# Kernel optimization log

Measured on AMD Instinct MI355X. Metric: run time of the kernel, lower is better.

## Reference

```python
import jax, jax.numpy as jnp
import numpy as np

B, LX, LY, D = 8, 128, 512, 256


def setup_inputs() -> dict:
    key = jax.random.key(0)
    k = jax.random.split(key, 7)
    s1 = 1.0 / np.sqrt(2 * D)
    s2 = 1.0 / np.sqrt(D)
    return {
        "x": jax.random.normal(k[0], (B, LX, D), dtype=jnp.float32),
        "y": jax.random.normal(k[1], (B, LY, D), dtype=jnp.float32),
        "y_mask": jax.random.randint(k[2], (B, LY), 0, 2).astype(bool),
        "W1": jax.random.uniform(k[3], (2 * D, D), jnp.float32, -s1, s1),
        "b1": jax.random.uniform(k[4], (D,), jnp.float32, -s1, s1),
        "W2": jax.random.uniform(k[5], (D, 1), jnp.float32, -s2, s2),
        "b2": jax.random.uniform(k[6], (1,), jnp.float32, -s2, s2),
    }


def reference(x, y, y_mask, W1, b1, W2, b2):
    # Algebraically split the first linear on the concat [x; y]:
    # cat([x,y]) @ W1 == x @ W1[:D] + y @ W1[D:]
    d = x.shape[-1]
    hx = jnp.einsum('bxd,de->bxe', x, W1[:d])            # (B, LX, D)
    hy = jnp.einsum('byd,de->bye', y, W1[d:])            # (B, LY, D)
    h = jax.nn.relu(hx[:, :, None, :] + hy[:, None, :, :] + b1)  # (B, LX, LY, D)
    scores = jnp.einsum('bxyd,d->bxy', h, W2[:, 0]) + b2[0]      # (B, LX, LY)
    scores = jnp.where(y_mask[:, None, :], -jnp.inf, scores)
    weights = jax.nn.softmax(scores, axis=2)
    contexts = jnp.einsum('bxy,byd->bxd', weights, y)    # (B, LX, D)
    return contexts
```

## Files before the change

### kernel.cpp

```cpp
#include <hip/hip_runtime.h>
#include <math.h>

#define BB 8
#define LX 128
#define LY 512
#define DD 256

typedef _Float16 h2t __attribute__((ext_vector_type(2)));

static __device__ __forceinline__ h2t u2h(unsigned int u) {
    h2t r; __builtin_memcpy(&r, &u, 4); return r;
}
static __device__ __forceinline__ unsigned int pk16(float a, float b) {
    h2t h; h.x = (_Float16)a; h.y = (_Float16)b;
    unsigned int u; __builtin_memcpy(&u, &h, 4); return u;
}

#if defined(__has_builtin) && __has_builtin(__builtin_amdgcn_fdot2)
#define DOT2(a, b, c) __builtin_amdgcn_fdot2((a), (b), (c), false)
#else
#define DOT2(a, b, c) fmaf((float)(a).x, (float)(b).x, fmaf((float)(a).y, (float)(b).y, (c)))
#endif

#define A16_OFF  0
#define CT16_OFF 131072
#define W16_OFF  655360
#define PART_OFF 655488
#define PML_OFF  4849792

__global__ __launch_bounds__(256) void gemm_kernel(
    const float* __restrict__ x, const float* __restrict__ y,
    const float* __restrict__ W1, const float* __restrict__ b1,
    const float* __restrict__ W2, float* __restrict__ ws)
{
    __shared__ float sA[32][20];
    __shared__ float sW[32][128];

    const int g  = blockIdx.x;
    const int t  = threadIdx.x;
    const int tc = t & 31;
    const int tr = t >> 5;

    const bool isA = (g < 128);
    const float* inp;
    const float* wbase;
    int row0, col0;
    if (isA) { col0 = (g & 1) * 128;  row0 = (g >> 1) * 16;  inp = x; wbase = W1; }
    else     { int h = g - 128; col0 = (h & 1) * 128; row0 = (h >> 1) * 16; inp = y; wbase = W1 + DD * DD; }

    float acc[2][4];
    #pragma unroll
    for (int i = 0; i < 2; ++i)
        #pragma unroll
        for (int j = 0; j < 4; ++j) acc[i][j] = 0.f;

    for (int k0 = 0; k0 < DD; k0 += 32) {
        __syncthreads();
        if (t < 128) {
            int row = t >> 3, kq = t & 7;
            const float4 v = *(const float4*)(inp + (size_t)(row0 + row) * DD + k0 + 4 * kq);
            sA[4*kq + 0][row] = v.x;
            sA[4*kq + 1][row] = v.y;
            sA[4*kq + 2][row] = v.z;
            sA[4*kq + 3][row] = v.w;
        }
        #pragma unroll
        for (int i = 0; i < 4; ++i) {
            int flat = t + i * 256;
            int kk = flat >> 5, c4 = flat & 31;
            *(float4*)&sW[kk][4*c4] = *(const float4*)(wbase + (size_t)(k0 + kk) * DD + col0 + 4 * c4);
        }
        __syncthreads();
        #pragma unroll
        for (int k = 0; k < 32; ++k) {
            const float a0 = sA[k][2*tr], a1 = sA[k][2*tr + 1];
            const float4 w4 = *(const float4*)&sW[k][4*tc];
            acc[0][0] = fmaf(a0, w4.x, acc[0][0]);
            acc[0][1] = fmaf(a0, w4.y, acc[0][1]);
            acc[0][2] = fmaf(a0, w4.z, acc[0][2]);
            acc[0][3] = fmaf(a0, w4.w, acc[0][3]);
            acc[1][0] = fmaf(a1, w4.x, acc[1][0]);
            acc[1][1] = fmaf(a1, w4.y, acc[1][1]);
            acc[1][2] = fmaf(a1, w4.z, acc[1][2]);
            acc[1][3] = fmaf(a1, w4.w, acc[1][3]);
        }
    }

    const int dq = (col0 >> 2) + tc;
    if (isA) {
        uint2* A16u2 = (uint2*)(ws + A16_OFF);
        const float4 bv = *(const float4*)(b1 + col0 + 4 * tc);
        #pragma unroll
        for (int i = 0; i < 2; ++i) {
            const int r = row0 + 2 * tr + i;
            uint2 st;
            st.x = pk16(acc[i][0] + bv.x, acc[i][1] + bv.y);
            st.y = pk16(acc[i][2] + bv.z, acc[i][3] + bv.w);
            A16u2[((size_t)r * 32 + (dq & 31)) * 2 + (dq >> 5)] = st;
        }
        if (g == 0 && t < 64) {
            uint2* W16u2 = (uint2*)(ws + W16_OFF);
            const float4 wv = *(const float4*)(W2 + 4 * t);
            uint2 st;
            st.x = pk16(wv.x, wv.y);
            st.y = pk16(wv.z, wv.w);
            W16u2[((t & 31)) * 2 + (t >> 5)] = st;
        }
    } else {
        uint2* Ct16u2 = (uint2*)(ws + CT16_OFF);
        #pragma unroll
        for (int i = 0; i < 2; ++i) {
            const int ry = row0 + 2 * tr + i;
            const int bb = ry >> 9, yy = ry & 511;
            uint2 st;
            st.x = pk16(acc[i][0], acc[i][1]);
            st.y = pk16(acc[i][2], acc[i][3]);
            Ct16u2[((size_t)(bb * 64 + dq)) * 512 + yy] = st;
        }
    }
}

__global__ __launch_bounds__(256) void score_kernel(
    const float* __restrict__ yin, const int* __restrict__ ymask,
    const float* __restrict__ b2,
    const uint4* __restrict__ A16, const uint2* __restrict__ Ct,
    const uint4* __restrict__ W16,
    float* __restrict__ part, float* __restrict__ pml)
{
    const int t    = threadIdx.x;
    const int lane = t & 63;
    const int w    = __builtin_amdgcn_readfirstlane(t >> 6);
    const int b    = blockIdx.x & 7;
    const int r2   = blockIdx.x >> 3;
    const int xg   = r2 & 15;
    const int yc   = r2 >> 4;
    const int ylo  = lane & 31;
    const bool hi  = (lane >> 5) != 0;
    const int y    = yc * 128 + w * 32 + ylo;
    const int grow0 = b * LX + xg * 8;

    const uint2* ctp = Ct + ((size_t)(b * 64 + (hi ? 32 : 0))) * 512 + y;
    const uint4* A8  = A16 + (size_t)grow0 * 32;
    const float  b2v = b2[0];

    h2t zz; zz.x = (_Float16)0.f; zz.y = (_Float16)0.f;
    float sA[8], sB[8];
    #pragma unroll
    for (int r = 0; r < 8; ++r) { sA[r] = 0.f; sB[r] = 0.f; }

    #pragma unroll 2
    for (int dqi = 0; dqi < 32; ++dqi) {
        const uint2 cu = ctp[(size_t)dqi * 512];
        const h2t c0 = u2h(cu.x), c1 = u2h(cu.y);
        const uint4 wv = W16[dqi];
        const h2t w0 = u2h(hi ? wv.z : wv.x);
        const h2t w1 = u2h(hi ? wv.w : wv.y);
        #pragma unroll
        for (int r = 0; r < 8; ++r) {
            const uint4 av = A8[r * 32 + dqi];
            const h2t a0 = u2h(hi ? av.z : av.x);
            const h2t a1 = u2h(hi ? av.w : av.y);
            const h2t h0 = __builtin_elementwise_max(a0 + c0, zz);
            const h2t h1 = __builtin_elementwise_max(a1 + c1, zz);
            sA[r] = DOT2(h0, w0, sA[r]);
            sB[r] = DOT2(h1, w1, sB[r]);
        }
    }

    const bool msk = ymask[(size_t)b * LY + y] != 0;
    float p[8]; int pi[8]; float l[8];
    #pragma unroll
    for (int r = 0; r < 8; ++r) {
        float s = sA[r] + sB[r];
        s += __shfl_xor(s, 32);
        p[r] = msk ? 0.f : __expf(s + b2v);
        pi[r] = __float_as_int(p[r]);
        float lv = p[r];
        #pragma unroll
        for (int off = 16; off; off >>= 1) lv += __shfl_xor(lv, off);
        l[r] = lv;
    }

    float4 acc[8];
    #pragma unroll
    for (int r = 0; r < 8; ++r) acc[r] = make_float4(0.f, 0.f, 0.f, 0.f);

    const float4* yb = (const float4*)yin + ((size_t)(b * LY + yc * 128 + w * 32)) * 64 + lane;
    #pragma unroll 4
    for (int yy = 0; yy < 32; ++yy) {
        const float4 v = yb[(size_t)yy * 64];
        #pragma unroll
        for (int r = 0; r < 8; ++r) {
            const float q = __int_as_float(__builtin_amdgcn_readlane(pi[r], yy));
            acc[r].x = fmaf(q, v.x, acc[r].x);
            acc[r].y = fmaf(q, v.y, acc[r].y);
            acc[r].z = fmaf(q, v.z, acc[r].z);
            acc[r].w = fmaf(q, v.w, acc[r].w);
        }
    }

    const size_t pw = (((size_t)(b * 16 + xg) * 4 + yc) * 4 + w);
    float* pb = part + pw * 8 * DD;
    #pragma unroll
    for (int r = 0; r < 8; ++r)
        *(float4*)(pb + (size_t)r * DD + 4 * lane) = acc[r];
    if (lane == 0) {
        #pragma unroll
        for (int r = 0; r < 8; ++r) pml[pw * 8 + r] = l[r];
    }
}

__global__ __launch_bounds__(256) void combine_kernel(
    const float* __restrict__ part, const float* __restrict__ pml,
    float* __restrict__ out)
{
    const int t = threadIdx.x;
    const int b = blockIdx.x & 7;
    const int x = blockIdx.x >> 3;
    const int xg = x >> 3, xi = x & 7;

    float L = 0.f;
    float acc = 0.f;
    #pragma unroll
    for (int c = 0; c < 16; ++c) {
        const size_t idx = (((size_t)(b * 16 + xg) * 4 + (c >> 2)) * 4 + (c & 3)) * 8 + xi;
        L   += pml[idx];
        acc += part[idx * DD + t];
    }
    out[((size_t)(b * LX + x)) * DD + t] = acc / L;
}

extern "C" void kernel_launch(void* const* d_in, const int* in_sizes, int n_in,
                              void* d_out, int out_size, void* d_ws, size_t ws_size,
                              hipStream_t stream) {
    const float* x     = (const float*)d_in[0];
    const float* y     = (const float*)d_in[1];
    const int*   ymask = (const int*)  d_in[2];
    const float* W1    = (const float*)d_in[3];
    const float* b1    = (const float*)d_in[4];
    const float* W2    = (const float*)d_in[5];
    const float* b2    = (const float*)d_in[6];
    float* ws  = (float*)d_ws;
    float* out = (float*)d_out;

    hipLaunchKernelGGL(gemm_kernel, dim3(640), dim3(256), 0, stream, x, y, W1, b1, W2, ws);
    hipLaunchKernelGGL(score_kernel, dim3(512), dim3(256), 0, stream,
                       y, ymask, b2,
                       (const uint4*)(ws + A16_OFF), (const uint2*)(ws + CT16_OFF),
                       (const uint4*)(ws + W16_OFF),
                       ws + PART_OFF, ws + PML_OFF);
    hipLaunchKernelGGL(combine_kernel, dim3(1024), dim3(256), 0, stream,
                       ws + PART_OFF, ws + PML_OFF, out);
}
```

Baseline: 50.41 us.

## Fuse score and combine kernels into one block-per-x-group kernel with LDS softmax weights

Replaces the split score/combine kernels with a single kernel in which each 512-thread block handles 4 query rows against all 512 y positions of one batch. A and W2 values are broadcast with readlane instead of per-row loads, and the A16/W16 layouts are simplified to match. Softmax weights are staged in LDS so the same block computes the weighted sum of y directly. This removes the partial-sum workspace traffic and one kernel launch. In exchange each block does a full-length 512-step reduction over y with 256 blocks, so there is less parallelism and more y reloads per block.

New measurement: 46.08 us. 1.09x faster.

```diff
diff --git a/kernel.cpp b/kernel.cpp
--- a/kernel.cpp
+++ b/kernel.cpp
@@ -14,6 +14,9 @@
 static __device__ __forceinline__ unsigned int pk16(float a, float b) {
     h2t h; h.x = (_Float16)a; h.y = (_Float16)b;
     unsigned int u; __builtin_memcpy(&u, &h, 4); return u;
+}
+static __device__ __forceinline__ h2t rlh(unsigned int v, int l) {
+    return u2h((unsigned int)__builtin_amdgcn_readlane((int)v, l));
 }
 
 #if defined(__has_builtin) && __has_builtin(__builtin_amdgcn_fdot2)
@@ -25,8 +28,6 @@
 #define A16_OFF  0
 #define CT16_OFF 131072
 #define W16_OFF  655360
-#define PART_OFF 655488
-#define PML_OFF  4849792
 
 __global__ __launch_bounds__(256) void gemm_kernel(
     const float* __restrict__ x, const float* __restrict__ y,
@@ -96,7 +97,7 @@
             uint2 st;
             st.x = pk16(acc[i][0] + bv.x, acc[i][1] + bv.y);
             st.y = pk16(acc[i][2] + bv.z, acc[i][3] + bv.w);
-            A16u2[((size_t)r * 32 + (dq & 31)) * 2 + (dq >> 5)] = st;
+            A16u2[(size_t)r * 64 + dq] = st;
         }
         if (g == 0 && t < 64) {
             uint2* W16u2 = (uint2*)(ws + W16_OFF);
@@ -104,7 +105,7 @@
             uint2 st;
             st.x = pk16(wv.x, wv.y);
             st.y = pk16(wv.z, wv.w);
-            W16u2[((t & 31)) * 2 + (t >> 5)] = st;
+            W16u2[t] = st;
         }
     } else {
         uint2* Ct16u2 = (uint2*)(ws + CT16_OFF);
@@ -120,114 +121,109 @@
     }
 }
 
-__global__ __launch_bounds__(256) void score_kernel(
+__global__ __launch_bounds__(512) void fused_kernel(
     const float* __restrict__ yin, const int* __restrict__ ymask,
     const float* __restrict__ b2,
-    const uint4* __restrict__ A16, const uint2* __restrict__ Ct,
-    const uint4* __restrict__ W16,
-    float* __restrict__ part, float* __restrict__ pml)
+    const uint2* __restrict__ A16, const uint2* __restrict__ Ct,
+    const uint2* __restrict__ W16,
+    float* __restrict__ out)
 {
+    __shared__ __align__(16) float pl[LY][4];
+    __shared__ __align__(16) float4 Lp[8];
+
     const int t    = threadIdx.x;
     const int lane = t & 63;
     const int w    = __builtin_amdgcn_readfirstlane(t >> 6);
     const int b    = blockIdx.x & 7;
-    const int r2   = blockIdx.x >> 3;
-    const int xg   = r2 & 15;
-    const int yc   = r2 >> 4;
-    const int ylo  = lane & 31;
-    const bool hi  = (lane >> 5) != 0;
-    const int y    = yc * 128 + w * 32 + ylo;
-    const int grow0 = b * LX + xg * 8;
-
-    const uint2* ctp = Ct + ((size_t)(b * 64 + (hi ? 32 : 0))) * 512 + y;
-    const uint4* A8  = A16 + (size_t)grow0 * 32;
+    const int xg   = blockIdx.x >> 3;
+    const int y    = w * 64 + lane;
+
+    const uint2* Ab = A16 + ((size_t)(b * LX + xg * 4)) * 64;
+    uint2 av0 = Ab[lane];
+    uint2 av1 = Ab[64 + lane];
+    uint2 av2 = Ab[128 + lane];
+    uint2 av3 = Ab[192 + lane];
+    const uint2 wv = W16[lane];
+
+    const uint2* ctb = Ct + ((size_t)b * 64) * 512 + y;
     const float  b2v = b2[0];
-
-    h2t zz; zz.x = (_Float16)0.f; zz.y = (_Float16)0.f;
-    float sA[8], sB[8];
+    const bool   msk = ymask[(size_t)b * LY + y] != 0;
+
+    float s0 = 0.f, s1 = 0.f, s2 = 0.f, s3 = 0.f;
+
+    #pragma unroll 4
+    for (int dq = 0; dq < 64; ++dq) {
+        const uint2 cu = ctb[(size_t)dq * 512];
+        const h2t c0 = u2h(cu.x), c1 = u2h(cu.y);
+        const h2t w0 = rlh(wv.x, dq), w1 = rlh(wv.y, dq);
+        h2t zz; zz.x = (_Float16)0.f; zz.y = (_Float16)0.f;
+        {
+            const h2t a0 = rlh(av0.x, dq), a1 = rlh(av0.y, dq);
+            const h2t h0 = __builtin_elementwise_max(a0 + c0, zz);
+            const h2t h1 = __builtin_elementwise_max(a1 + c1, zz);
+            s0 = DOT2(h0, w0, s0); s0 = DOT2(h1, w1, s0);
+        }
+        {
+            const h2t a0 = rlh(av1.x, dq), a1 = rlh(av1.y, dq);
+            const h2t h0 = __builtin_elementwise_max(a0 + c0, zz);
+            const h2t h1 = __builtin_elementwise_max(a1 + c1, zz);
+            s1 = DOT2(h0, w0, s1); s1 = DOT2(h1, w1, s1);
+        }
+        {
+            const h2t a0 = rlh(av2.x, dq), a1 = rlh(av2.y, dq);
+            const h2t h0 = __builtin_elementwise_max(a0 + c0, zz);
+            const h2t h1 = __builtin_elementwise_max(a1 + c1, zz);
+            s2 = DOT2(h0, w0, s2); s2 = DOT2(h1, w1, s2);
+        }
+        {
+            const h2t a0 = rlh(av3.x, dq), a1 = rlh(av3.y, dq);
+            const h2t h0 = __builtin_elementwise_max(a0 + c0, zz);
+            const h2t h1 = __builtin_elementwise_max(a1 + c1, zz);
+            s3 = DOT2(h0, w0, s3); s3 = DOT2(h1, w1, s3);
+        }
+    }
+
+    const float p0 = msk ? 0.f : __expf(s0 + b2v);
+    const float p1 = msk ? 0.f : __expf(s1 + b2v);
+    const float p2 = msk ? 0.f : __expf(s2 + b2v);
+    const float p3 = msk ? 0.f : __expf(s3 + b2v);
+
+    float l0 = p0, l1 = p1, l2 = p2, l3 = p3;
     #pragma unroll
-    for (int r = 0; r < 8; ++r) { sA[r] = 0.f; sB[r] = 0.f; }
-
-    #pragma unroll 2
-    for (int dqi = 0; dqi < 32; ++dqi) {
-        const uint2 cu = ctp[(size_t)dqi * 512];
-        const h2t c0 = u2h(cu.x), c1 = u2h(cu.y);
-        const uint4 wv = W16[dqi];
-        const h2t w0 = u2h(hi ? wv.z : wv.x);
-        const h2t w1 = u2h(hi ? wv.w : wv.y);
-        #pragma unroll
-        for (int r = 0; r < 8; ++r) {
-            const uint4 av = A8[r * 32 + dqi];
-            const h2t a0 = u2h(hi ? av.z : av.x);
-            const h2t a1 = u2h(hi ? av.w : av.y);
-            const h2t h0 = __builtin_elementwise_max(a0 + c0, zz);
-            const h2t h1 = __builtin_elementwise_max(a1 + c1, zz);
-            sA[r] = DOT2(h0, w0, sA[r]);
-            sB[r] = DOT2(h1, w1, sB[r]);
-        }
-    }
-
-    const bool msk = ymask[(size_t)b * LY + y] != 0;
-    float p[8]; int pi[8]; float l[8];
+    for (int off = 32; off; off >>= 1) {
+        l0 += __shfl_xor(l0, off);
+        l1 += __shfl_xor(l1, off);
+        l2 += __shfl_xor(l2, off);
+        l3 += __shfl_xor(l3, off);
+    }
+
+    *(float4*)&pl[y][0] = make_float4(p0, p1, p2, p3);
+    if (lane == 0) Lp[w] = make_float4(l0, l1, l2, l3);
+    __syncthreads();
+
+    const int d  = t & 255;
+    const int xh = t >> 8;
+    float L0 = 0.f, L1 = 0.f;
     #pragma unroll
-    for (int r = 0; r < 8; ++r) {
-        float s = sA[r] + sB[r];
-        s += __shfl_xor(s, 32);
-        p[r] = msk ? 0.f : __expf(s + b2v);
-        pi[r] = __float_as_int(p[r]);
-        float lv = p[r];
-        #pragma unroll
-        for (int off = 16; off; off >>= 1) lv += __shfl_xor(lv, off);
-        l[r] = lv;
-    }
-
-    float4 acc[8];
-    #pragma unroll
-    for (int r = 0; r < 8; ++r) acc[r] = make_float4(0.f, 0.f, 0.f, 0.f);
-
-    const float4* yb = (const float4*)yin + ((size_t)(b * LY + yc * 128 + w * 32)) * 64 + lane;
-    #pragma unroll 4
-    for (int yy = 0; yy < 32; ++yy) {
-        const float4 v = yb[(size_t)yy * 64];
-        #pragma unroll
-        for (int r = 0; r < 8; ++r) {
-            const float q = __int_as_float(__builtin_amdgcn_readlane(pi[r], yy));
-            acc[r].x = fmaf(q, v.x, acc[r].x);
-            acc[r].y = fmaf(q, v.y, acc[r].y);
-            acc[r].z = fmaf(q, v.z, acc[r].z);
-            acc[r].w = fmaf(q, v.w, acc[r].w);
-        }
-    }
-
-    const size_t pw = (((size_t)(b * 16 + xg) * 4 + yc) * 4 + w);
-    float* pb = part + pw * 8 * DD;
-    #pragma unroll
-    for (int r = 0; r < 8; ++r)
-        *(float4*)(pb + (size_t)r * DD + 4 * lane) = acc[r];
-    if (lane == 0) {
-        #pragma unroll
-        for (int r = 0; r < 8; ++r) pml[pw * 8 + r] = l[r];
-    }
-}
-
-__global__ __launch_bounds__(256) void combine_kernel(
-    const float* __restrict__ part, const float* __restrict__ pml,
-    float* __restrict__ out)
-{
-    const int t = threadIdx.x;
-    const int b = blockIdx.x & 7;
-    const int x = blockIdx.x >> 3;
-    const int xg = x >> 3, xi = x & 7;
-
-    float L = 0.f;
-    float acc = 0.f;
-    #pragma unroll
-    for (int c = 0; c < 16; ++c) {
-        const size_t idx = (((size_t)(b * 16 + xg) * 4 + (c >> 2)) * 4 + (c & 3)) * 8 + xi;
-        L   += pml[idx];
-        acc += part[idx * DD + t];
-    }
-    out[((size_t)(b * LX + x)) * DD + t] = acc / L;
+    for (int ww = 0; ww < 8; ++ww) {
+        const float4 lv = Lp[ww];
+        L0 += xh ? lv.z : lv.x;
+        L1 += xh ? lv.w : lv.y;
+    }
+
+    float a0 = 0.f, a1 = 0.f;
+    const float* Yb = yin + (size_t)b * LY * DD + d;
+    #pragma unroll 8
+    for (int yy = 0; yy < LY; ++yy) {
+        const float v = Yb[(size_t)yy * DD];
+        const float2 pp = *(const float2*)&pl[yy][2 * xh];
+        a0 = fmaf(pp.x, v, a0);
+        a1 = fmaf(pp.y, v, a1);
+    }
+
+    const size_t row = (size_t)(b * LX + xg * 4 + 2 * xh);
+    out[row * DD + d]       = a0 / L0;
+    out[(row + 1) * DD + d] = a1 / L1;
 }
 
 extern "C" void kernel_launch(void* const* d_in, const int* in_sizes, int n_in,
@@ -244,11 +240,8 @@
     float* out = (float*)d_out;
 
     hipLaunchKernelGGL(gemm_kernel, dim3(640), dim3(256), 0, stream, x, y, W1, b1, W2, ws);
-    hipLaunchKernelGGL(score_kernel, dim3(512), dim3(256), 0, stream,
+    hipLaunchKernelGGL(fused_kernel, dim3(256), dim3(512), 0, stream,
                        y, ymask, b2,
-                       (const uint4*)(ws + A16_OFF), (const uint2*)(ws + CT16_OFF),
-                       (const uint4*)(ws + W16_OFF),
-                       ws + PART_OFF, ws + PML_OFF);
-    hipLaunchKernelGGL(combine_kernel, dim3(1024), dim3(256), 0, stream,
-                       ws + PART_OFF, ws + PML_OFF, out);
-}
+                       (const uint2*)(ws + A16_OFF), (const uint2*)(ws + CT16_OFF),
+                       (const uint2*)(ws + W16_OFF), out);
+}
```
